# Performance work log

Measured on AMD Instinct MI355X. Metric: run time of the kernel, lower is better.

The kernel has to match this reference:

```python
import jax, jax.numpy as jnp
import numpy as np

TEMP = 0.07  # softmax temperature T


def _l2norm(x, axis=1, eps=1e-12):
    return x / jnp.clip(jnp.linalg.norm(x, axis=axis, keepdims=True), eps, None)


def setup_inputs() -> dict:
    key = jax.random.key(0)
    k1, k2, k3, k4 = jax.random.split(key, 4)
    B, K, D = 256, 8192, 128
    q = jax.random.normal(k1, (B, D), dtype=jnp.float32)
    ba_queue = _l2norm(jax.random.normal(k2, (K, D), dtype=jnp.float32))
    nonba_queue = _l2norm(jax.random.normal(k3, (K, D), dtype=jnp.float32))
    targets = jax.random.randint(k4, (B,), 0, 2, dtype=jnp.int64)
    return {"q": q, "ba_queue": ba_queue, "nonba_queue": nonba_queue, "targets": targets}


def reference(q, ba_queue, nonba_queue, targets):
    K = ba_queue.shape[0]
    # encoder output is L2-normalized; queues are detached buffers
    qn = _l2norm(q, axis=1)
    all_feature = jnp.concatenate([qn, ba_queue, nonba_queue], axis=0)  # [N, D]
    all_label = jnp.concatenate([
        targets.astype(jnp.int32),
        jnp.ones((K,), dtype=jnp.int32),
        jnp.zeros((K,), dtype=jnp.int32),
    ])  # [N]
    N = all_feature.shape[0]

    # [N, N] similarity logits
    sim = jnp.matmul(all_feature, all_feature.T) / TEMP
    logits = sim - jax.lax.stop_gradient(jnp.max(sim, axis=1, keepdims=True))

    # positive mask (same label), excluding self
    mask = (all_label[:, None] == all_label[None, :]).astype(jnp.float32)
    logits_mask = 1.0 - jnp.eye(N, dtype=jnp.float32)
    mask = mask * logits_mask

    exp_logits = jnp.exp(logits) * logits_mask
    log_prob = logits - jnp.log(jnp.sum(exp_logits, axis=1, keepdims=True))
    mean_log_prob_pos = jnp.sum(mask * log_prob, axis=1) / jnp.sum(mask, axis=1)
    return -jnp.mean(mean_log_prob_pos)
```

## Files before the change

### kernel.cpp

```cpp
#include <hip/hip_runtime.h>
#include <hip/hip_bf16.h>
#include <stdint.h>

#define TEMPERATURE 0.07f
#define SC 20.6099312f

constexpr int NQ = 256;
constexpr int KQ = 8192;
constexpr int D  = 128;
constexpr int N  = NQ + 2 * KQ;
constexpr int CSW = 52;
constexpr int NTW = 520 / CSW;
constexpr int RBF = N / 256;

typedef float f32x16 __attribute__((ext_vector_type(16)));
typedef int   i32x4  __attribute__((ext_vector_type(4)));
typedef int   i32x8  __attribute__((ext_vector_type(8)));

constexpr size_t OFF_F32  = 0;
constexpr size_t OFF_8    = OFF_F32  + (size_t)NQ * D * 4;
constexpr size_t OFF_8S   = OFF_8    + (size_t)N * D;
constexpr size_t OFF_PART = OFF_8S   + (size_t)N * D;
constexpr size_t OFF_LP   = OFF_PART + (size_t)CSW * N * 4;
constexpr size_t OFF_BSUM = OFF_LP   + (size_t)260 * 2 * 128 * 4;

#define MFMA8(a, b, c) __builtin_amdgcn_mfma_scale_f32_32x32x64_f8f6f4( \
    (a), (b), (c), 0, 0, 0, 0x7f7f7f7f, 0, 0x7f7f7f7f)

__global__ __launch_bounds__(256) void k_prep(const float* __restrict__ q,
                                              const float* __restrict__ ba,
                                              const float* __restrict__ nb,
                                              const long long* __restrict__ tgt,
                                              float* __restrict__ ff,
                                              unsigned char* __restrict__ fb8,
                                              unsigned char* __restrict__ fb8s,
                                              float* __restrict__ lp) {
    __shared__ float red[4][2][128];
    int wid = threadIdx.x >> 6, lane = threadIdx.x & 63;
    int rbase = blockIdx.x * 64 + wid * 16;
    float s0x = 0.f, s0y = 0.f, s1x = 0.f, s1y = 0.f;
    for (int i = 0; i < 16; ++i) {
        int r = rbase + i;
        const float* src = (r < NQ) ? (q + (size_t)r * D)
                         : (r < NQ + KQ) ? (ba + (size_t)(r - NQ) * D)
                         : (nb + (size_t)(r - NQ - KQ) * D);
        float2 v = *(const float2*)(src + lane * 2);
        float a = v.x, b = v.y;
        int lab;
        if (r < NQ) {
            float ss = a * a + b * b;
            #pragma unroll
            for (int m = 1; m < 64; m <<= 1) ss += __shfl_xor(ss, m);
            float scale = 1.0f / fmaxf(sqrtf(ss), 1e-12f);
            a *= scale; b *= scale;
            lab = (int)tgt[r];
            *(float2*)(ff + (size_t)r * D + lane * 2) = make_float2(a, b);
        } else {
            lab = (r < NQ + KQ) ? 1 : 0;
        }
        int w8  = __builtin_amdgcn_cvt_pk_fp8_f32(a, b, 0, false);
        int w8s = __builtin_amdgcn_cvt_pk_fp8_f32(a * SC, b * SC, 0, false);
        *(unsigned short*)(fb8  + (size_t)r * D + lane * 2) = (unsigned short)w8;
        *(unsigned short*)(fb8s + (size_t)r * D + lane * 2) = (unsigned short)w8s;
        if (lab) { s1x += a; s1y += b; } else { s0x += a; s0y += b; }
    }
    red[wid][0][lane * 2]     = s0x;
    red[wid][0][lane * 2 + 1] = s0y;
    red[wid][1][lane * 2]     = s1x;
    red[wid][1][lane * 2 + 1] = s1y;
    __syncthreads();
    int lab2 = threadIdx.x >> 7, d = threadIdx.x & 127;
    float s = red[0][lab2][d] + red[1][lab2][d] + red[2][lab2][d] + red[3][lab2][d];
    lp[((size_t)blockIdx.x * 2 + lab2) * 128 + d] = s;
}

__global__ __launch_bounds__(256, 4) void k_main(const unsigned char* __restrict__ fb8,
                                                 const unsigned char* __restrict__ fb8s,
                                                 float* __restrict__ part) {
    __shared__ __align__(16) unsigned char lds[4][2][4096];
    const int tid = threadIdx.x;
    const int lane = tid & 63;
    const int wid  = tid >> 6;
    const int job  = blockIdx.x * 4 + wid;
    const int rg = job / CSW, cs = job % CSW;
    const int l31 = lane & 31, lhi = lane >> 5;
    const int rw = rg * 64;

    unsigned char* myl = &lds[wid][0][0];

    int soff[4];
    #pragma unroll
    for (int i = 0; i < 4; ++i) {
        int f = i * 64 + lane;
        int row = f >> 3, pslot = f & 7;
        soff[i] = row * 128 + ((pslot ^ (row & 7)) << 4);
    }
    int lofs[2][2];
    #pragma unroll
    for (int s = 0; s < 2; ++s) {
        int p = s * 4 + lhi * 2;
        lofs[s][0] = (l31 * 8 + ((p)     ^ (l31 & 7))) * 16;
        lofs[s][1] = (l31 * 8 + ((p + 1) ^ (l31 & 7))) * 16;
    }

#define STAGE(T, B) { \
    const unsigned char* base_ = fb8 + ((size_t)(cs + (T) * CSW)) * 4096; \
    _Pragma("unroll") \
    for (int i_ = 0; i_ < 4; ++i_) \
        __builtin_amdgcn_global_load_lds( \
            (const __attribute__((address_space(1))) unsigned int*)(base_ + soff[i_]), \
            (__attribute__((address_space(3))) unsigned int*)(myl + (B) * 4096 + (i_ * 64 + lane) * 16), \
            16, 0, 0); }

    i32x8 rf[2][2];
    #pragma unroll
    for (int rs = 0; rs < 2; ++rs)
        #pragma unroll
        for (int s = 0; s < 2; ++s)
            rf[rs][s] = *(const i32x8*)(fb8s + (size_t)(rw + rs * 32 + l31) * D + s * 64 + lhi * 32);

    f32x16 z16;
    #pragma unroll
    for (int e = 0; e < 16; ++e) z16[e] = 0.f;

    float2 ps2[2] = {{0.f, 0.f}, {0.f, 0.f}};

    STAGE(0, 0)

    #pragma unroll 1
    for (int t = 0; t < NTW; ++t) {
        if (t + 1 < NTW) {
            STAGE(t + 1, (t & 1) ^ 1)
            asm volatile("s_waitcnt vmcnt(4)" ::: "memory");
        } else {
            asm volatile("s_waitcnt vmcnt(0)" ::: "memory");
        }
        const unsigned char* buf = myl + (t & 1) * 4096;

        f32x16 acc[2];
        __builtin_amdgcn_s_setprio(1);
        #pragma unroll
        for (int s = 0; s < 2; ++s) {
            i32x4 lo = *(const i32x4*)(buf + lofs[s][0]);
            i32x4 hi = *(const i32x4*)(buf + lofs[s][1]);
            i32x8 a = {lo[0], lo[1], lo[2], lo[3], hi[0], hi[1], hi[2], hi[3]};
            acc[0] = MFMA8(a, rf[0][s], (s == 0) ? z16 : acc[0]);
            acc[1] = MFMA8(a, rf[1][s], (s == 0) ? z16 : acc[1]);
        }
        __builtin_amdgcn_s_setprio(0);

        #pragma unroll
        for (int rs = 0; rs < 2; ++rs) {
            float2 p = {0.f, 0.f};
            #pragma unroll
            for (int g = 0; g < 8; ++g) {
                p.x += __builtin_amdgcn_exp2f(acc[rs][2 * g]);
                p.y += __builtin_amdgcn_exp2f(acc[rs][2 * g + 1]);
            }
            ps2[rs].x += p.x; ps2[rs].y += p.y;
        }
    }

    float rsum0 = ps2[0].x + ps2[0].y;
    float rsum1 = ps2[1].x + ps2[1].y;
    rsum0 += __shfl_xor(rsum0, 32);
    rsum1 += __shfl_xor(rsum1, 32);
    if (lane < 32) {
        part[(size_t)cs * N + rw + lane]      = rsum0;
        part[(size_t)cs * N + rw + 32 + lane] = rsum1;
    }
#undef STAGE
}

__global__ __launch_bounds__(256) void k_rowfin(const float* __restrict__ part,
                                                const float* __restrict__ ff,
                                                const float* __restrict__ ba,
                                                const float* __restrict__ nb,
                                                const float* __restrict__ lp,
                                                const long long* __restrict__ tgt,
                                                float* __restrict__ bsum) {
    __shared__ float sS[256];
    __shared__ float red[256];
    __shared__ int scnt[2];
    {
        int lab = threadIdx.x >> 7, d = threadIdx.x & 127;
        float s[4] = {0.f, 0.f, 0.f, 0.f};
        for (int b = 0; b < 260; b += 4) {
            #pragma unroll
            for (int j = 0; j < 4; ++j)
                s[j] += lp[((size_t)(b + j) * 2 + lab) * 128 + d];
        }
        sS[threadIdx.x] = (s[0] + s[1]) + (s[2] + s[3]);
        if (threadIdx.x < 64) {
            int c = 0;
            #pragma unroll
            for (int i = 0; i < 4; ++i) c += (int)tgt[threadIdx.x + 64 * i];
            #pragma unroll
            for (int m = 1; m < 64; m <<= 1) c += __shfl_xor(c, m);
            if (threadIdx.x == 0) { scnt[0] = (NQ - c) + KQ; scnt[1] = c + KQ; }
        }
    }
    __syncthreads();
    int r = blockIdx.x * 256 + threadIdx.x;
    float se = 0.f;
    #pragma unroll 4
    for (int c = 0; c < CSW; ++c) se += part[(size_t)c * N + r];
    int lab = (r < NQ) ? (int)tgt[r] : ((r < NQ + KQ) ? 1 : 0);
    const float* fsrc = (r < NQ) ? (ff + (size_t)r * D)
                      : (r < NQ + KQ) ? (ba + (size_t)(r - NQ) * D)
                      : (nb + (size_t)(r - NQ - KQ) * D);
    const float4* frow = (const float4*)fsrc;
    const float4* srow = (const float4*)(sS + lab * 128);
    float dS = 0.f, dd = 0.f;
    #pragma unroll
    for (int i = 0; i < 32; ++i) {
        float4 f = frow[i];
        float4 s = srow[i];
        dS += f.x * s.x + f.y * s.y + f.z * s.z + f.w * s.w;
        int wa  = __builtin_amdgcn_cvt_pk_fp8_f32(f.x, f.y, 0, false);
        int wb  = __builtin_amdgcn_cvt_pk_fp8_f32(f.z, f.w, 0, false);
        int wsa = __builtin_amdgcn_cvt_pk_fp8_f32(f.x * SC, f.y * SC, 0, false);
        int wsb = __builtin_amdgcn_cvt_pk_fp8_f32(f.z * SC, f.w * SC, 0, false);
        dd += __builtin_amdgcn_cvt_f32_fp8(wa, 0) * __builtin_amdgcn_cvt_f32_fp8(wsa, 0)
            + __builtin_amdgcn_cvt_f32_fp8(wa, 1) * __builtin_amdgcn_cvt_f32_fp8(wsa, 1)
            + __builtin_amdgcn_cvt_f32_fp8(wb, 0) * __builtin_amdgcn_cvt_f32_fp8(wsb, 0)
            + __builtin_amdgcn_cvt_f32_fp8(wb, 1) * __builtin_amdgcn_cvt_f32_fp8(wsb, 1);
    }
    se -= __builtin_amdgcn_exp2f(dd);
    float lse = logf(se);
    float P = (float)(scnt[lab] - 1);
    float mlpp = (dS - 1.0f) / (TEMPERATURE * P) - lse;
    red[threadIdx.x] = mlpp;
    __syncthreads();
    for (int s2 = 128; s2 > 0; s2 >>= 1) {
        if (threadIdx.x < s2) red[threadIdx.x] += red[threadIdx.x + s2];
        __syncthreads();
    }
    if (threadIdx.x == 0) bsum[blockIdx.x] = red[0];
}

__global__ __launch_bounds__(64) void k_final(const float* __restrict__ bsum,
                                              float* __restrict__ out) {
    float s = bsum[threadIdx.x];
    if (threadIdx.x == 0) s += bsum[64];
    #pragma unroll
    for (int m = 1; m < 64; m <<= 1) s += __shfl_xor(s, m);
    if (threadIdx.x == 0) out[0] = -s / (float)N;
}

extern "C" void kernel_launch(void* const* d_in, const int* in_sizes, int n_in,
                              void* d_out, int out_size, void* d_ws, size_t ws_size,
                              hipStream_t stream) {
    const float* q       = (const float*)d_in[0];
    const float* ba      = (const float*)d_in[1];
    const float* nb      = (const float*)d_in[2];
    const long long* tgt = (const long long*)d_in[3];
    char* ws = (char*)d_ws;
    float*         ff   = (float*)(ws + OFF_F32);
    unsigned char* fb8  = (unsigned char*)(ws + OFF_8);
    unsigned char* fb8s = (unsigned char*)(ws + OFF_8S);
    float*         part = (float*)(ws + OFF_PART);
    float*         lp   = (float*)(ws + OFF_LP);
    float*         bsum = (float*)(ws + OFF_BSUM);

    k_prep  <<<260,  256, 0, stream>>>(q, ba, nb, tgt, ff, fb8, fb8s, lp);
    k_main  <<<3380, 256, 0, stream>>>(fb8, fb8s, part);
    k_rowfin<<<RBF,  256, 0, stream>>>(part, ff, ba, nb, lp, tgt, bsum);
    k_final <<<1,     64, 0, stream>>>(bsum, (float*)d_out);
}
```

Measured before the change: 87.57 us.

## Exploit Gram matrix symmetry to compute only lower-triangular tiles

Since the similarity matrix is symmetric, each tile now computes only the lower-triangular blocks. The exp sums from each tile feed both row partials and column partials, and the column sums are reduced through LDS. The aim is to roughly halve the MFMA and exp2 work in the main kernel. The cost is extra column-reduction work, a larger partial-sum buffer with a longer reduction in rowfin, and load imbalance across waves, many of which exit early.

```diff
diff --git a/kernel.cpp b/kernel.cpp
--- a/kernel.cpp
+++ b/kernel.cpp
@@ -9,8 +9,8 @@
 constexpr int KQ = 8192;
 constexpr int D  = 128;
 constexpr int N  = NQ + 2 * KQ;
-constexpr int CSW = 52;
-constexpr int NTW = 520 / CSW;
+constexpr int NSTRIP = 260;
+constexpr int NCH = 52;
 constexpr int RBF = N / 256;
 
 typedef float f32x16 __attribute__((ext_vector_type(16)));
@@ -20,8 +20,9 @@
 constexpr size_t OFF_F32  = 0;
 constexpr size_t OFF_8    = OFF_F32  + (size_t)NQ * D * 4;
 constexpr size_t OFF_8S   = OFF_8    + (size_t)N * D;
-constexpr size_t OFF_PART = OFF_8S   + (size_t)N * D;
-constexpr size_t OFF_LP   = OFF_PART + (size_t)CSW * N * 4;
+constexpr size_t OFF_PR   = OFF_8S   + (size_t)N * D;
+constexpr size_t OFF_PC   = OFF_PR   + (size_t)NSTRIP * N * 4;
+constexpr size_t OFF_LP   = OFF_PC   + (size_t)NCH * N * 4;
 constexpr size_t OFF_BSUM = OFF_LP   + (size_t)260 * 2 * 128 * 4;
 
 #define MFMA8(a, b, c) __builtin_amdgcn_mfma_scale_f32_32x32x64_f8f6f4( \
@@ -76,35 +77,48 @@
 
 __global__ __launch_bounds__(256, 4) void k_main(const unsigned char* __restrict__ fb8,
                                                  const unsigned char* __restrict__ fb8s,
-                                                 float* __restrict__ part) {
-    __shared__ __align__(16) unsigned char lds[4][2][4096];
+                                                 float* __restrict__ part_row,
+                                                 float* __restrict__ part_col) {
+    __shared__ __align__(16) unsigned char lds[4][8192];
     const int tid = threadIdx.x;
     const int lane = tid & 63;
     const int wid  = tid >> 6;
-    const int job  = blockIdx.x * 4 + wid;
-    const int rg = job / CSW, cs = job % CSW;
+    const int slot = blockIdx.x + 3380 * wid;
+    const int J  = slot % NSTRIP;
+    const int ch = slot / NSTRIP;
+    const int nt0   = ch * 10;
+    const int ntend = min(nt0 + 10, 2 * J + 2);
+    if (nt0 >= ntend) return;
     const int l31 = lane & 31, lhi = lane >> 5;
-    const int rw = rg * 64;
-
-    unsigned char* myl = &lds[wid][0][0];
+
+    unsigned char* myl = &lds[wid][0];
+
+    i32x8 af[2][2];
+    #pragma unroll
+    for (int cc = 0; cc < 2; ++cc)
+        #pragma unroll
+        for (int s = 0; s < 2; ++s)
+            af[cc][s] = *(const i32x8*)(fb8s + (size_t)(64 * J + cc * 32 + l31) * D + s * 64 + lhi * 32);
 
     int soff[4];
     #pragma unroll
     for (int i = 0; i < 4; ++i) {
-        int f = i * 64 + lane;
-        int row = f >> 3, pslot = f & 7;
-        soff[i] = row * 128 + ((pslot ^ (row & 7)) << 4);
+        int flat = i * 64 + lane;
+        int line = flat >> 4, sl = flat & 15;
+        int pl = sl ^ line;
+        soff[i] = (2 * line + (pl >> 3)) * 128 + (pl & 7) * 16;
     }
     int lofs[2][2];
     #pragma unroll
     for (int s = 0; s < 2; ++s) {
-        int p = s * 4 + lhi * 2;
-        lofs[s][0] = (l31 * 8 + ((p)     ^ (l31 & 7))) * 16;
-        lofs[s][1] = (l31 * 8 + ((p + 1) ^ (l31 & 7))) * 16;
-    }
-
-#define STAGE(T, B) { \
-    const unsigned char* base_ = fb8 + ((size_t)(cs + (T) * CSW)) * 4096; \
+        int line = l31 >> 1;
+        int p = ((l31 & 1) << 3) + s * 4 + lhi * 2;
+        lofs[s][0] = line * 256 + ((p    ) ^ line) * 16;
+        lofs[s][1] = line * 256 + ((p + 1) ^ line) * 16;
+    }
+
+#define STAGE(NT, B) { \
+    const unsigned char* base_ = fb8 + (size_t)(NT) * 4096; \
     _Pragma("unroll") \
     for (int i_ = 0; i_ < 4; ++i_) \
         __builtin_amdgcn_global_load_lds( \
@@ -112,67 +126,76 @@
             (__attribute__((address_space(3))) unsigned int*)(myl + (B) * 4096 + (i_ * 64 + lane) * 16), \
             16, 0, 0); }
 
-    i32x8 rf[2][2];
-    #pragma unroll
-    for (int rs = 0; rs < 2; ++rs)
-        #pragma unroll
-        for (int s = 0; s < 2; ++s)
-            rf[rs][s] = *(const i32x8*)(fb8s + (size_t)(rw + rs * 32 + l31) * D + s * 64 + lhi * 32);
-
-    f32x16 z16;
-    #pragma unroll
-    for (int e = 0; e < 16; ++e) z16[e] = 0.f;
-
-    float2 ps2[2] = {{0.f, 0.f}, {0.f, 0.f}};
-
-    STAGE(0, 0)
-
-    #pragma unroll 1
-    for (int t = 0; t < NTW; ++t) {
-        if (t + 1 < NTW) {
-            STAGE(t + 1, (t & 1) ^ 1)
+    f32x16 z16, cA, cB;
+    #pragma unroll
+    for (int e = 0; e < 16; ++e) { z16[e] = 0.f; cA[e] = 0.f; cB[e] = 0.f; }
+
+    STAGE(nt0, 0)
+
+    for (int nt = nt0; nt < ntend; ++nt) {
+        int b = (nt - nt0) & 1;
+        if (nt + 1 < ntend) {
+            STAGE(nt + 1, b ^ 1)
             asm volatile("s_waitcnt vmcnt(4)" ::: "memory");
         } else {
             asm volatile("s_waitcnt vmcnt(0)" ::: "memory");
         }
-        const unsigned char* buf = myl + (t & 1) * 4096;
-
-        f32x16 acc[2];
+        const unsigned char* buf = myl + b * 4096;
+
+        f32x16 acc0, acc1;
         __builtin_amdgcn_s_setprio(1);
         #pragma unroll
         for (int s = 0; s < 2; ++s) {
             i32x4 lo = *(const i32x4*)(buf + lofs[s][0]);
             i32x4 hi = *(const i32x4*)(buf + lofs[s][1]);
-            i32x8 a = {lo[0], lo[1], lo[2], lo[3], hi[0], hi[1], hi[2], hi[3]};
-            acc[0] = MFMA8(a, rf[0][s], (s == 0) ? z16 : acc[0]);
-            acc[1] = MFMA8(a, rf[1][s], (s == 0) ? z16 : acc[1]);
+            i32x8 bb = {lo[0], lo[1], lo[2], lo[3], hi[0], hi[1], hi[2], hi[3]};
+            acc0 = MFMA8(af[0][s], bb, (s == 0) ? z16 : acc0);
+            acc1 = MFMA8(af[1][s], bb, (s == 0) ? z16 : acc1);
         }
         __builtin_amdgcn_s_setprio(0);
 
-        #pragma unroll
-        for (int rs = 0; rs < 2; ++rs) {
-            float2 p = {0.f, 0.f};
-            #pragma unroll
-            for (int g = 0; g < 8; ++g) {
-                p.x += __builtin_amdgcn_exp2f(acc[rs][2 * g]);
-                p.y += __builtin_amdgcn_exp2f(acc[rs][2 * g + 1]);
+        float rowp = 0.f;
+        if (nt < 2 * J) {
+            #pragma unroll
+            for (int g = 0; g < 16; ++g) {
+                float e0 = __builtin_amdgcn_exp2f(acc0[g]);
+                float e1 = __builtin_amdgcn_exp2f(acc1[g]);
+                rowp += e0 + e1;
+                cA[g] += e0; cB[g] += e1;
             }
-            ps2[rs].x += p.x; ps2[rs].y += p.y;
-        }
-    }
-
-    float rsum0 = ps2[0].x + ps2[0].y;
-    float rsum1 = ps2[1].x + ps2[1].y;
-    rsum0 += __shfl_xor(rsum0, 32);
-    rsum1 += __shfl_xor(rsum1, 32);
-    if (lane < 32) {
-        part[(size_t)cs * N + rw + lane]      = rsum0;
-        part[(size_t)cs * N + rw + 32 + lane] = rsum1;
-    }
+        } else {
+            #pragma unroll
+            for (int g = 0; g < 16; ++g)
+                rowp += __builtin_amdgcn_exp2f(acc0[g]) + __builtin_amdgcn_exp2f(acc1[g]);
+        }
+        rowp += __shfl_xor(rowp, 32);
+        if (lane < 32)
+            part_row[(size_t)J * N + 32 * nt + l31] = rowp;
+    }
+
+    #pragma unroll
+    for (int j4 = 0; j4 < 4; ++j4) {
+        float4 vA = {cA[j4 * 4 + 0], cA[j4 * 4 + 1], cA[j4 * 4 + 2], cA[j4 * 4 + 3]};
+        float4 vB = {cB[j4 * 4 + 0], cB[j4 * 4 + 1], cB[j4 * 4 + 2], cB[j4 * 4 + 3]};
+        *(float4*)(myl + lane * 128 + ((j4    ) ^ (lane & 7)) * 16) = vA;
+        *(float4*)(myl + lane * 128 + ((j4 + 4) ^ (lane & 7)) * 16) = vB;
+    }
+    asm volatile("s_waitcnt lgkmcnt(0)" ::: "memory");
+    int lhij = (lane >> 2) & 1;
+    int slj  = ((lane >> 5) << 4) | (lane & 3) | (((lane >> 3) & 3) << 2);
+    float csum = 0.f;
+    #pragma unroll 8
+    for (int s2 = 0; s2 < 32; ++s2) {
+        int srcr = s2 + (lhij << 5);
+        int phys = (slj >> 2) ^ (s2 & 7);
+        csum += *(const float*)(myl + srcr * 128 + phys * 16 + (slj & 3) * 4);
+    }
+    part_col[(size_t)ch * N + 64 * J + lane] = csum;
 #undef STAGE
 }
 
-__global__ __launch_bounds__(256) void k_rowfin(const float* __restrict__ part,
+__global__ __launch_bounds__(256) void k_rowfin(const float* __restrict__ part_row,
+                                                const float* __restrict__ part_col,
                                                 const float* __restrict__ ff,
                                                 const float* __restrict__ ba,
                                                 const float* __restrict__ nb,
@@ -202,9 +225,11 @@
     }
     __syncthreads();
     int r = blockIdx.x * 256 + threadIdx.x;
+    int J0 = r >> 6;
     float se = 0.f;
-    #pragma unroll 4
-    for (int c = 0; c < CSW; ++c) se += part[(size_t)c * N + r];
+    for (int Jx = J0; Jx < NSTRIP; ++Jx) se += part_row[(size_t)Jx * N + r];
+    int nch = (2 * J0 + 1) / 10 + 1;
+    for (int c2 = 0; c2 < nch; ++c2) se += part_col[(size_t)c2 * N + r];
     int lab = (r < NQ) ? (int)tgt[r] : ((r < NQ + KQ) ? 1 : 0);
     const float* fsrc = (r < NQ) ? (ff + (size_t)r * D)
                       : (r < NQ + KQ) ? (ba + (size_t)(r - NQ) * D)
@@ -259,12 +284,13 @@
     float*         ff   = (float*)(ws + OFF_F32);
     unsigned char* fb8  = (unsigned char*)(ws + OFF_8);
     unsigned char* fb8s = (unsigned char*)(ws + OFF_8S);
-    float*         part = (float*)(ws + OFF_PART);
+    float*         pr   = (float*)(ws + OFF_PR);
+    float*         pc   = (float*)(ws + OFF_PC);
     float*         lp   = (float*)(ws + OFF_LP);
     float*         bsum = (float*)(ws + OFF_BSUM);
 
     k_prep  <<<260,  256, 0, stream>>>(q, ba, nb, tgt, ff, fb8, fb8s, lp);
-    k_main  <<<3380, 256, 0, stream>>>(fb8, fb8s, part);
-    k_rowfin<<<RBF,  256, 0, stream>>>(part, ff, ba, nb, lp, tgt, bsum);
+    k_main  <<<3380, 256, 0, stream>>>(fb8, fb8s, pr, pc);
+    k_rowfin<<<RBF,  256, 0, stream>>>(pr, pc, ff, ba, nb, lp, tgt, bsum);
     k_final <<<1,     64, 0, stream>>>(bsum, (float*)d_out);
 }
```

Result: slower. 171.3 us (+95.6%).
